# Performance work log

Hardware: AMD Instinct MI355X
Metric: run time of the kernel (lower is better)

Reference implementation:

```python
import jax, jax.numpy as jnp
import numpy as np

B = 8        # graphs per batch
VG = 20000   # vertices per graph
K = 128      # eigenvectors per graph
D = 128      # channels (C_inout)
V = B * VG


def setup_inputs() -> dict:
    key = jax.random.key(0)
    kx, km, ke, kv, kt = jax.random.split(key, 5)
    x = jax.random.normal(kx, (V, D), dtype=jnp.float32)
    # lumped (diagonal) mass, positive
    mass = jax.random.uniform(km, (V,), dtype=jnp.float32, minval=0.5, maxval=1.5)
    # per-graph nonnegative eigenvalues, sorted within each graph, stacked to (B*K,)
    evals = jnp.sort(jax.random.uniform(ke, (B, K), dtype=jnp.float32) * 10.0, axis=1).reshape(-1)
    # eigenbasis, roughly mass-orthonormal scale
    evecs = jax.random.normal(kv, (V, K), dtype=jnp.float32) / np.sqrt(VG)
    # learned per-channel diffusion times, positive
    diffusion_time = jax.random.uniform(kt, (D,), dtype=jnp.float32, minval=0.01, maxval=0.2)
    batch = jnp.repeat(jnp.arange(B, dtype=jnp.int32), VG)
    return {"x": x, "mass": mass, "evals": evals, "evecs": evecs,
            "diffusion_time": diffusion_time, "batch": batch, "bs": B}


def reference(x, mass, evals, evecs, diffusion_time, batch, bs):
    Vtot, Dc = x.shape
    neig = evals.shape[0] // bs
    vg = Vtot // bs  # equal-sized graphs -> ragged grouped matmul == batched matmul
    t = jnp.maximum(diffusion_time, 1e-8)  # torch clamp(min=1e-8)
    xb = x.reshape(bs, vg, Dc)            # (B, Vg, D)
    eb = evecs.reshape(bs, vg, neig)      # (B, Vg, K)
    mb = mass.reshape(bs, vg)             # (B, Vg) diagonal mass
    # to_basis: basis^T @ (M x) per graph -> (B, K, D)
    x_spec = jnp.einsum('bvk,bvd->bkd', eb * mb[..., None], xb)
    # spectral diffusion coefficients exp(-lambda * t_c): (B, K, D)
    coefs = jnp.exp(-evals.reshape(bs, neig)[..., None] * t[None, None, :])
    # from_basis: evecs @ (coefs * x_spec) per graph -> (B, Vg, D)
    x_diffuse = jnp.einsum('bvk,bkd->bvd', eb, coefs * x_spec)
    return x_diffuse.reshape(Vtot, Dc)
```

## Files before the change

kernel.cpp:

```cpp
#include <hip/hip_runtime.h>

#define BGR 8
#define VG  20000
#define NK  128
#define ND  128

typedef float f32x4 __attribute__((ext_vector_type(4)));
typedef short bf16x8 __attribute__((ext_vector_type(8)));

__device__ __forceinline__ unsigned cvtpk(float a, float b) {
    unsigned r;
    asm("v_cvt_pk_bf16_f32 %0, %1, %2" : "=v"(r) : "v"(a), "v"(b));
    return r;
}

#define VC 320
#define S1 40

__global__ __launch_bounds__(256) void k_spec(const float* __restrict__ x,
                                              const float* __restrict__ mass,
                                              const float* __restrict__ evecs,
                                              float* __restrict__ xsT) {
    const int g     = blockIdx.y;
    const int chunk = blockIdx.x;
    const int v0    = chunk * VC;
    const int nv    = (VG - v0 < VC) ? (VG - v0) : VC;
    const int rounds = nv >> 5;

    const float* xg = x     + (size_t)g * VG * ND;
    const float* eg = evecs + (size_t)g * VG * NK;
    const float* mg = mass  + (size_t)g * VG;

    __shared__ short Et[NK * S1];
    __shared__ short Xt[ND * S1];

    const int tid = threadIdx.x;
    const int l   = tid & 63;
    const int w   = tid >> 6;
    const int lo  = l & 15, hi = l >> 4;
    const int r0  = (w & 1) * 64, c0 = (w >> 1) * 64;

    const int cc = l;
    const int oc = w;

    float eA[8], eB[8], xA[8], xB[8], mm[8];

    auto loadr = [&](int r) {
        const int vb = v0 + r * 32 + oc * 8;
#pragma unroll
        for (int q = 0; q < 8; ++q) {
            const size_t re = (size_t)(vb + q) * NK;
            const size_t rx = (size_t)(vb + q) * ND;
            eA[q] = eg[re + cc];  eB[q] = eg[re + cc + 64];
            xA[q] = xg[rx + cc];  xB[q] = xg[rx + cc + 64];
            mm[q] = mg[vb + q];
        }
    };

    f32x4 acc[4][4] = {};
    loadr(0);

    for (int r = 0; r < rounds; ++r) {
        uint4 u;
        u.x = cvtpk(eA[0], eA[1]); u.y = cvtpk(eA[2], eA[3]);
        u.z = cvtpk(eA[4], eA[5]); u.w = cvtpk(eA[6], eA[7]);
        *(uint4*)(Et + cc * S1 + oc * 8) = u;
        u.x = cvtpk(eB[0], eB[1]); u.y = cvtpk(eB[2], eB[3]);
        u.z = cvtpk(eB[4], eB[5]); u.w = cvtpk(eB[6], eB[7]);
        *(uint4*)(Et + (cc + 64) * S1 + oc * 8) = u;
        u.x = cvtpk(xA[0] * mm[0], xA[1] * mm[1]); u.y = cvtpk(xA[2] * mm[2], xA[3] * mm[3]);
        u.z = cvtpk(xA[4] * mm[4], xA[5] * mm[5]); u.w = cvtpk(xA[6] * mm[6], xA[7] * mm[7]);
        *(uint4*)(Xt + cc * S1 + oc * 8) = u;
        u.x = cvtpk(xB[0] * mm[0], xB[1] * mm[1]); u.y = cvtpk(xB[2] * mm[2], xB[3] * mm[3]);
        u.z = cvtpk(xB[4] * mm[4], xB[5] * mm[5]); u.w = cvtpk(xB[6] * mm[6], xB[7] * mm[7]);
        *(uint4*)(Xt + (cc + 64) * S1 + oc * 8) = u;

        if (r + 1 < rounds) loadr(r + 1);
        __syncthreads();

        bf16x8 ax[4], be[4];
#pragma unroll
        for (int i = 0; i < 4; ++i)
            ax[i] = *(const bf16x8*)(Xt + (r0 + 16 * i + lo) * S1 + hi * 8);
#pragma unroll
        for (int j = 0; j < 4; ++j)
            be[j] = *(const bf16x8*)(Et + (c0 + 16 * j + lo) * S1 + hi * 8);
#pragma unroll
        for (int i = 0; i < 4; ++i)
#pragma unroll
            for (int j = 0; j < 4; ++j)
                acc[i][j] = __builtin_amdgcn_mfma_f32_16x16x32_bf16(ax[i], be[j], acc[i][j], 0, 0, 0);
        __syncthreads();
    }

    float* og = xsT + (size_t)g * ND * NK;
#pragma unroll
    for (int i = 0; i < 4; ++i)
#pragma unroll
        for (int j = 0; j < 4; ++j)
#pragma unroll
            for (int t = 0; t < 4; ++t) {
                const int dd = r0 + 16 * i + hi * 4 + t;
                const int kk = c0 + 16 * j + lo;
                atomicAdd(og + dd * NK + kk, acc[i][j][t]);
            }
}

__global__ __launch_bounds__(256) void k_coef(const float* __restrict__ xsT,
                                              const float* __restrict__ evals,
                                              const float* __restrict__ dt,
                                              short* __restrict__ Yt) {
    const int q  = blockIdx.x * 256 + threadIdx.x;
    const int g  = q >> 12;
    const int d  = (q >> 5) & 127;
    const int k4 = (q & 31) << 2;
    const float t = fmaxf(dt[d], 1e-8f);
    const float4 lam = *(const float4*)(evals + g * NK + k4);
    const float4 v   = *(const float4*)(xsT + (size_t)g * ND * NK + d * NK + k4);
    uint2 r;
    r.x = cvtpk(__expf(-lam.x * t) * v.x, __expf(-lam.y * t) * v.y);
    r.y = cvtpk(__expf(-lam.z * t) * v.z, __expf(-lam.w * t) * v.w);
    *(uint2*)(Yt + (size_t)g * ND * NK + d * NK + k4) = r;
}

__global__ __launch_bounds__(256) void k_out(const float* __restrict__ evecs,
                                             const short* __restrict__ Yt,
                                             float* __restrict__ out) {
    const int g     = blockIdx.y;
    const int chunk = blockIdx.x;
    const int v0    = chunk * 128;
    const int rows  = (VG - v0 < 128) ? (VG - v0) : 128;

    const float* eg = evecs + (size_t)g * VG * NK;
    float*       og = out   + (size_t)g * VG * ND;
    const short* yg = Yt    + (size_t)g * ND * NK;

    __shared__ short As[128 * 128];
    __shared__ short Bs[128 * 128];

    const int tid = threadIdx.x;

#pragma unroll
    for (int it = 0; it < 16; ++it) {
        const int id = it * 256 + tid;
        const int v  = id >> 5;
        const int c4 = (id & 31) << 2;
        const int vc = v < rows ? v : rows - 1;
        const float4 e4 = *(const float4*)(eg + (size_t)(v0 + vc) * NK + c4);
        uint2 p; p.x = cvtpk(e4.x, e4.y); p.y = cvtpk(e4.z, e4.w);
        *(uint2*)(As + v * 128 + (((c4 >> 3) ^ (v & 7)) << 3) + (c4 & 7)) = p;
        if (it < 8) {
            const int s16 = it * 256 + tid;
            const int rr  = s16 >> 4, gq = s16 & 15;
            *(uint4*)(Bs + rr * 128 + ((gq ^ (rr & 7)) << 3)) =
                *(const uint4*)(yg + s16 * 8);
        }
    }
    __syncthreads();

    const int l  = tid & 63;
    const int w  = tid >> 6;
    const int lo = l & 15, hi = l >> 4;
    const int r0 = (w & 1) * 64, c0 = (w >> 1) * 64;

    f32x4 acc[4][4] = {};
#pragma unroll
    for (int ks = 0; ks < 4; ++ks) {
        bf16x8 af[4], bv[4];
#pragma unroll
        for (int i = 0; i < 4; ++i) {
            const int R = r0 + 16 * i + lo;
            af[i] = *(const bf16x8*)(As + R * 128 + ((((ks << 2) + hi) ^ (R & 7)) << 3));
        }
#pragma unroll
        for (int j = 0; j < 4; ++j) {
            const int Dd = c0 + 16 * j + lo;
            bv[j] = *(const bf16x8*)(Bs + Dd * 128 + ((((ks << 2) + hi) ^ (Dd & 7)) << 3));
        }
#pragma unroll
        for (int i = 0; i < 4; ++i)
#pragma unroll
            for (int j = 0; j < 4; ++j)
                acc[i][j] = __builtin_amdgcn_mfma_f32_16x16x32_bf16(af[i], bv[j], acc[i][j], 0, 0, 0);
    }

#pragma unroll
    for (int i = 0; i < 4; ++i)
#pragma unroll
        for (int j = 0; j < 4; ++j)
#pragma unroll
            for (int t = 0; t < 4; ++t) {
                const int vv = r0 + 16 * i + hi * 4 + t;
                if (vv < rows)
                    og[(size_t)(v0 + vv) * ND + c0 + 16 * j + lo] = acc[i][j][t];
            }
}

extern "C" void kernel_launch(void* const* d_in, const int* in_sizes, int n_in,
                              void* d_out, int out_size, void* d_ws, size_t ws_size,
                              hipStream_t stream) {
    const float* x     = (const float*)d_in[0];
    const float* mass  = (const float*)d_in[1];
    const float* evals = (const float*)d_in[2];
    const float* evecs = (const float*)d_in[3];
    const float* dt    = (const float*)d_in[4];
    float* out = (float*)d_out;

    float* xsT = (float*)d_ws;
    short* Yt  = (short*)((char*)d_ws + (size_t)BGR * ND * NK * 4);

    hipMemsetAsync(d_ws, 0, (size_t)BGR * ND * NK * sizeof(float), stream);

    k_spec<<<dim3((VG + VC - 1) / VC, BGR), 256, 0, stream>>>(x, mass, evecs, xsT);
    k_coef<<<(BGR * ND * NK / 4) / 256, 256, 0, stream>>>(xsT, evals, dt, Yt);
    k_out<<<dim3((VG + 127) / 128, BGR), 256, 0, stream>>>(evecs, Yt, out);
}
```

Baseline: 259.7 us.

## Replace atomic reduction with scratch partials and persist k_out with double-buffered tiles

k_spec now uses smaller vertex chunks (160) with a fully unrolled loop. Each block writes its partial spectral tile to scratch space inside the output buffer instead of doing atomicAdd, which also removes the memset. k_coef sums the 125 partials per graph before applying the exp coefficients. k_out becomes a persistent kernel: 64 slots per graph walk 64-row evec tiles with register prefetch and a double-buffered LDS tile, so global loads overlap the MFMA work. The costs are extra scratch traffic and a serial reduction loop in k_coef.

```diff
diff --git a/kernel.cpp b/kernel.cpp
--- a/kernel.cpp
+++ b/kernel.cpp
@@ -14,18 +14,24 @@
     return r;
 }
 
-#define VC 320
-#define S1 40
+__device__ __forceinline__ short bf16r(float f) {
+    union { float f; unsigned u; } c; c.f = f;
+    unsigned r = (c.u + 0x7FFFu + ((c.u >> 16) & 1u)) >> 16;
+    return (short)r;
+}
+
+#define VC  160
+#define S1  40
+#define NCH (VG / VC)
 
 __global__ __launch_bounds__(256) void k_spec(const float* __restrict__ x,
                                               const float* __restrict__ mass,
                                               const float* __restrict__ evecs,
-                                              float* __restrict__ xsT) {
-    const int g     = blockIdx.y;
-    const int chunk = blockIdx.x;
+                                              float* __restrict__ scr) {
+    const int bid   = blockIdx.x;
+    const int g     = bid & 7;
+    const int chunk = bid >> 3;
     const int v0    = chunk * VC;
-    const int nv    = (VG - v0 < VC) ? (VG - v0) : VC;
-    const int rounds = nv >> 5;
 
     const float* xg = x     + (size_t)g * VG * ND;
     const float* eg = evecs + (size_t)g * VG * NK;
@@ -60,7 +66,8 @@
     f32x4 acc[4][4] = {};
     loadr(0);
 
-    for (int r = 0; r < rounds; ++r) {
+#pragma unroll
+    for (int r = 0; r < VC / 32; ++r) {
         uint4 u;
         u.x = cvtpk(eA[0], eA[1]); u.y = cvtpk(eA[2], eA[3]);
         u.z = cvtpk(eA[4], eA[5]); u.w = cvtpk(eA[6], eA[7]);
@@ -75,7 +82,7 @@
         u.z = cvtpk(xB[4] * mm[4], xB[5] * mm[5]); u.w = cvtpk(xB[6] * mm[6], xB[7] * mm[7]);
         *(uint4*)(Xt + (cc + 64) * S1 + oc * 8) = u;
 
-        if (r + 1 < rounds) loadr(r + 1);
+        if (r + 1 < VC / 32) loadr(r + 1);
         __syncthreads();
 
         bf16x8 ax[4], be[4];
@@ -93,7 +100,7 @@
         __syncthreads();
     }
 
-    float* og = xsT + (size_t)g * ND * NK;
+    float* sg = scr + (size_t)bid * ND * NK;
 #pragma unroll
     for (int i = 0; i < 4; ++i)
 #pragma unroll
@@ -102,98 +109,135 @@
             for (int t = 0; t < 4; ++t) {
                 const int dd = r0 + 16 * i + hi * 4 + t;
                 const int kk = c0 + 16 * j + lo;
-                atomicAdd(og + dd * NK + kk, acc[i][j][t]);
+                sg[dd * NK + kk] = acc[i][j][t];
             }
 }
 
-__global__ __launch_bounds__(256) void k_coef(const float* __restrict__ xsT,
+__global__ __launch_bounds__(256) void k_coef(const float* __restrict__ scr,
                                               const float* __restrict__ evals,
                                               const float* __restrict__ dt,
                                               short* __restrict__ Yt) {
-    const int q  = blockIdx.x * 256 + threadIdx.x;
-    const int g  = q >> 12;
-    const int d  = (q >> 5) & 127;
-    const int k4 = (q & 31) << 2;
+    const int q   = blockIdx.x * 256 + threadIdx.x;
+    const int g   = q >> 14;
+    const int rem = q & 16383;
+    const int d   = rem >> 7;
+    const int k   = rem & 127;
+    const float* p = scr + (size_t)g * ND * NK + rem;
+    float s = 0.f;
+#pragma unroll 25
+    for (int c = 0; c < NCH; ++c)
+        s += p[(size_t)c * 8 * ND * NK];
     const float t = fmaxf(dt[d], 1e-8f);
-    const float4 lam = *(const float4*)(evals + g * NK + k4);
-    const float4 v   = *(const float4*)(xsT + (size_t)g * ND * NK + d * NK + k4);
-    uint2 r;
-    r.x = cvtpk(__expf(-lam.x * t) * v.x, __expf(-lam.y * t) * v.y);
-    r.y = cvtpk(__expf(-lam.z * t) * v.z, __expf(-lam.w * t) * v.w);
-    *(uint2*)(Yt + (size_t)g * ND * NK + d * NK + k4) = r;
-}
+    Yt[q] = bf16r(__expf(-evals[g * NK + k] * t) * s);
+}
+
+#define TV  64
+#define NT  ((VG + TV - 1) / TV)
+#define NSL 64
 
 __global__ __launch_bounds__(256) void k_out(const float* __restrict__ evecs,
                                              const short* __restrict__ Yt,
                                              float* __restrict__ out) {
-    const int g     = blockIdx.y;
-    const int chunk = blockIdx.x;
-    const int v0    = chunk * 128;
-    const int rows  = (VG - v0 < 128) ? (VG - v0) : 128;
+    const int bid  = blockIdx.x;
+    const int g    = bid & 7;
+    const int slot = bid >> 3;
 
     const float* eg = evecs + (size_t)g * VG * NK;
     float*       og = out   + (size_t)g * VG * ND;
     const short* yg = Yt    + (size_t)g * ND * NK;
 
-    __shared__ short As[128 * 128];
     __shared__ short Bs[128 * 128];
+    __shared__ short As[2][TV * 128];
 
     const int tid = threadIdx.x;
 
 #pragma unroll
-    for (int it = 0; it < 16; ++it) {
-        const int id = it * 256 + tid;
-        const int v  = id >> 5;
-        const int c4 = (id & 31) << 2;
-        const int vc = v < rows ? v : rows - 1;
-        const float4 e4 = *(const float4*)(eg + (size_t)(v0 + vc) * NK + c4);
-        uint2 p; p.x = cvtpk(e4.x, e4.y); p.y = cvtpk(e4.z, e4.w);
-        *(uint2*)(As + v * 128 + (((c4 >> 3) ^ (v & 7)) << 3) + (c4 & 7)) = p;
-        if (it < 8) {
-            const int s16 = it * 256 + tid;
-            const int rr  = s16 >> 4, gq = s16 & 15;
-            *(uint4*)(Bs + rr * 128 + ((gq ^ (rr & 7)) << 3)) =
-                *(const uint4*)(yg + s16 * 8);
+    for (int it = 0; it < 8; ++it) {
+        const int s16 = it * 256 + tid;
+        const int rr  = s16 >> 4, gq = s16 & 15;
+        *(uint4*)(Bs + rr * 128 + ((gq ^ (rr & 7)) << 3)) =
+            *(const uint4*)(yg + s16 * 8);
+    }
+
+    const int vrow = tid >> 2;
+    const int q4   = tid & 3;
+
+    float4 ld[8];
+    auto load_tile = [&](int t) {
+        const int tv0  = t * TV;
+        const int rows = (VG - tv0 < TV) ? (VG - tv0) : TV;
+        const int vc   = vrow < rows ? vrow : rows - 1;
+        const float* src = eg + (size_t)(tv0 + vc) * NK + q4 * 32;
+#pragma unroll
+        for (int f = 0; f < 8; ++f) ld[f] = *(const float4*)(src + 4 * f);
+    };
+    auto write_tile = [&](int buf) {
+        short* A = As[buf];
+#pragma unroll
+        for (int h = 0; h < 4; ++h) {
+            uint4 u;
+            u.x = cvtpk(ld[2 * h].x, ld[2 * h].y);
+            u.y = cvtpk(ld[2 * h].z, ld[2 * h].w);
+            u.z = cvtpk(ld[2 * h + 1].x, ld[2 * h + 1].y);
+            u.w = cvtpk(ld[2 * h + 1].z, ld[2 * h + 1].w);
+            const int g8 = q4 * 4 + h;
+            *(uint4*)(A + vrow * 128 + ((g8 ^ (vrow & 7)) << 3)) = u;
         }
-    }
-    __syncthreads();
+    };
 
     const int l  = tid & 63;
     const int w  = tid >> 6;
     const int lo = l & 15, hi = l >> 4;
-    const int r0 = (w & 1) * 64, c0 = (w >> 1) * 64;
-
-    f32x4 acc[4][4] = {};
-#pragma unroll
-    for (int ks = 0; ks < 4; ++ks) {
-        bf16x8 af[4], bv[4];
-#pragma unroll
-        for (int i = 0; i < 4; ++i) {
-            const int R = r0 + 16 * i + lo;
-            af[i] = *(const bf16x8*)(As + R * 128 + ((((ks << 2) + hi) ^ (R & 7)) << 3));
+    const int r0 = (w & 1) * 32, c0 = (w >> 1) * 64;
+
+    int t = slot;
+    load_tile(t);
+    write_tile(0);
+    int cur = 0;
+
+    for (; t < NT; t += NSL) {
+        const int tn = t + NSL;
+        if (tn < NT) load_tile(tn);
+        __syncthreads();
+
+        f32x4 acc[2][4] = {};
+        const short* A = As[cur];
+#pragma unroll
+        for (int ks = 0; ks < 4; ++ks) {
+            bf16x8 af[2], bv[4];
+#pragma unroll
+            for (int i = 0; i < 2; ++i) {
+                const int R = r0 + 16 * i + lo;
+                af[i] = *(const bf16x8*)(A + R * 128 + ((((ks << 2) + hi) ^ (R & 7)) << 3));
+            }
+#pragma unroll
+            for (int j = 0; j < 4; ++j) {
+                const int Dd = c0 + 16 * j + lo;
+                bv[j] = *(const bf16x8*)(Bs + Dd * 128 + ((((ks << 2) + hi) ^ (Dd & 7)) << 3));
+            }
+#pragma unroll
+            for (int i = 0; i < 2; ++i)
+#pragma unroll
+                for (int j = 0; j < 4; ++j)
+                    acc[i][j] = __builtin_amdgcn_mfma_f32_16x16x32_bf16(af[i], bv[j], acc[i][j], 0, 0, 0);
         }
-#pragma unroll
-        for (int j = 0; j < 4; ++j) {
-            const int Dd = c0 + 16 * j + lo;
-            bv[j] = *(const bf16x8*)(Bs + Dd * 128 + ((((ks << 2) + hi) ^ (Dd & 7)) << 3));
-        }
-#pragma unroll
-        for (int i = 0; i < 4; ++i)
+
+        const int tv0  = t * TV;
+        const int rows = (VG - tv0 < TV) ? (VG - tv0) : TV;
+#pragma unroll
+        for (int i = 0; i < 2; ++i)
 #pragma unroll
             for (int j = 0; j < 4; ++j)
-                acc[i][j] = __builtin_amdgcn_mfma_f32_16x16x32_bf16(af[i], bv[j], acc[i][j], 0, 0, 0);
+#pragma unroll
+                for (int u = 0; u < 4; ++u) {
+                    const int vv = r0 + 16 * i + hi * 4 + u;
+                    if (vv < rows)
+                        og[(size_t)(tv0 + vv) * ND + c0 + 16 * j + lo] = acc[i][j][u];
+                }
+
+        if (tn < NT) write_tile(cur ^ 1);
+        cur ^= 1;
     }
-
-#pragma unroll
-    for (int i = 0; i < 4; ++i)
-#pragma unroll
-        for (int j = 0; j < 4; ++j)
-#pragma unroll
-            for (int t = 0; t < 4; ++t) {
-                const int vv = r0 + 16 * i + hi * 4 + t;
-                if (vv < rows)
-                    og[(size_t)(v0 + vv) * ND + c0 + 16 * j + lo] = acc[i][j][t];
-            }
 }
 
 extern "C" void kernel_launch(void* const* d_in, const int* in_sizes, int n_in,
@@ -206,12 +250,10 @@
     const float* dt    = (const float*)d_in[4];
     float* out = (float*)d_out;
 
-    float* xsT = (float*)d_ws;
-    short* Yt  = (short*)((char*)d_ws + (size_t)BGR * ND * NK * 4);
-
-    hipMemsetAsync(d_ws, 0, (size_t)BGR * ND * NK * sizeof(float), stream);
-
-    k_spec<<<dim3((VG + VC - 1) / VC, BGR), 256, 0, stream>>>(x, mass, evecs, xsT);
-    k_coef<<<(BGR * ND * NK / 4) / 256, 256, 0, stream>>>(xsT, evals, dt, Yt);
-    k_out<<<dim3((VG + 127) / 128, BGR), 256, 0, stream>>>(evecs, Yt, out);
-}
+    float* scr = out;
+    short* Yt  = (short*)d_ws;
+
+    k_spec<<<NCH * BGR, 256, 0, stream>>>(x, mass, evecs, scr);
+    k_coef<<<(BGR * ND * NK) / 256, 256, 0, stream>>>(scr, evals, dt, Yt);
+    k_out<<<NSL * BGR, 256, 0, stream>>>(evecs, Yt, out);
+}
```

New measurement: 252.4 us. 1.03x faster.
